# Performance work log

Hardware: AMD Instinct MI355X
Metric: run time of the kernel (lower is better)

## Reference

```python
import jax, jax.numpy as jnp
import numpy as np

N_NODES = 50000
N_EDGES = 800000
IN_CH = 256
HID = 512
NUM_LAYERS = 3
EPS = 1e-12  # F.normalize eps


def setup_inputs() -> dict:
    key = jax.random.key(0)
    ks = jax.random.split(key, 2 + 3 * NUM_LAYERS)
    x = jax.random.normal(ks[0], (N_NODES, IN_CH), dtype=jnp.float32)
    edge_index = jax.random.randint(ks[1], (2, N_EDGES), 0, N_NODES, dtype=jnp.int64)
    inp = {"x": x, "edge_index": edge_index}
    dims = [(IN_CH, HID)] + [(HID, HID)] * (NUM_LAYERS - 1)
    for i, (din, dout) in enumerate(dims):
        s = 1.0 / np.sqrt(din)
        inp[f"Wl{i}"] = jax.random.normal(ks[2 + 3 * i], (din, dout), dtype=jnp.float32) * s
        inp[f"bl{i}"] = jnp.zeros((dout,), dtype=jnp.float32)
        inp[f"Wr{i}"] = jax.random.normal(ks[3 + 3 * i], (din, dout), dtype=jnp.float32) * s
    return inp


def _sage_conv(x, src, dst, Wl, bl, Wr):
    # aggr='add': out[dst] += x[src], then lin_l(agg) + lin_r(x), L2 normalize rows
    agg = jax.ops.segment_sum(x[src], dst, num_segments=x.shape[0])  # [N, din]
    out = agg @ Wl + bl + x @ Wr  # [N, dout]
    norm = jnp.maximum(jnp.linalg.norm(out, axis=-1, keepdims=True), EPS)
    return out / norm


def reference(x, edge_index, Wl0, bl0, Wr0, Wl1, bl1, Wr1, Wl2, bl2, Wr2):
    src, dst = edge_index[0], edge_index[1]
    feat = x
    params = [(Wl0, bl0, Wr0), (Wl1, bl1, Wr1), (Wl2, bl2, Wr2)]
    for Wl, bl, Wr in params:
        aggre = _sage_conv(feat, src, dst, Wl, bl, Wr)
        # Dropout(p=0.15) is identity in eval mode
        feat = jax.nn.elu(aggre)
    return feat
```

## Files before the change

kernel.cpp:

```cpp
#include <hip/hip_runtime.h>
#include <math.h>

#define N_NODES 50000
#define M_PAD   50048
#define N_EDGES 800000
#define HID 512

typedef short bf16x8 __attribute__((ext_vector_type(8)));
typedef float f32x4  __attribute__((ext_vector_type(4)));
typedef unsigned short u16x4 __attribute__((ext_vector_type(4)));
typedef unsigned short u16x8 __attribute__((ext_vector_type(8)));

__device__ inline float b2f(unsigned short u) {
    union { unsigned int i; float f; } v; v.i = ((unsigned int)u) << 16; return v.f;
}
__device__ inline unsigned short f2b(float f) {
    union { float f; unsigned int i; } v; v.f = f;
    unsigned int r = v.i + 0x7FFFu + ((v.i >> 16) & 1u);
    return (unsigned short)(r >> 16);
}


__global__ void zero_kernel(int* __restrict__ p, int n) {
    int i = blockIdx.x * blockDim.x + threadIdx.x;
    if (i < n) p[i] = 0;
}

__global__ void detect_kernel(const int* __restrict__ e, int* __restrict__ flag) {
    if (blockIdx.x == 0 && threadIdx.x == 0) {
        int is64 = 1;
        for (int i = 0; i < 16; ++i)
            if (e[2 * i + 1] != 0) is64 = 0;
        *flag = is64;
    }
}

__global__ void hist_kernel(const void* __restrict__ eidx, const int* __restrict__ flag,
                            int* __restrict__ counts) {
    int e = blockIdx.x * blockDim.x + threadIdx.x;
    if (e >= N_EDGES) return;
    int is64 = *flag;
    int d;
    if (is64) d = (int)((const long long*)eidx)[N_EDGES + e];
    else      d = ((const int*)eidx)[N_EDGES + e];
    atomicAdd(&counts[d], 1);
}

__global__ __launch_bounds__(1024) void scan_kernel(const int* __restrict__ counts,
                                                    int* __restrict__ offsets) {
    __shared__ int sums[1024];
    int t = threadIdx.x;
    const int CH = (N_NODES + 1023) / 1024;
    int lo = t * CH;
    int hi = min(lo + CH, N_NODES);
    int s = 0;
    for (int i = lo; i < hi; ++i) s += counts[i];
    sums[t] = s;
    __syncthreads();
    for (int off = 1; off < 1024; off <<= 1) {
        int v = 0;
        if (t >= off) v = sums[t - off];
        __syncthreads();
        sums[t] += v;
        __syncthreads();
    }
    int excl = (t == 0) ? 0 : sums[t - 1];
    for (int i = lo; i < hi; ++i) { offsets[i] = excl; excl += counts[i]; }
    if (t == 1023) offsets[N_NODES] = excl;
}

__global__ void fill_kernel(const void* __restrict__ eidx, const int* __restrict__ flag,
                            const int* __restrict__ offsets, int* __restrict__ cursor,
                            int* __restrict__ edge_src) {
    int e = blockIdx.x * blockDim.x + threadIdx.x;
    if (e >= N_EDGES) return;
    int is64 = *flag;
    int s, d;
    if (is64) {
        const long long* p = (const long long*)eidx;
        s = (int)p[e];
        d = (int)p[N_EDGES + e];
    } else {
        const int* p = (const int*)eidx;
        s = p[e];
        d = p[N_EDGES + e];
    }
    int pos = atomicAdd(&cursor[d], 1);
    edge_src[offsets[d] + pos] = s;
}


__global__ __launch_bounds__(256) void xconv_kernel(const float* __restrict__ x,
                                                    unsigned short* __restrict__ cat1) {
    int id = blockIdx.x * 256 + threadIdx.x;
    if (id >= M_PAD * 64) return;
    int row = id >> 6;
    int c = (id & 63) * 4;
    float4 v = make_float4(0.f, 0.f, 0.f, 0.f);
    if (row < N_NODES) v = *(const float4*)(x + (size_t)row * 256 + c);
    ushort4 h;
    h.x = f2b(v.x); h.y = f2b(v.y); h.z = f2b(v.z); h.w = f2b(v.w);
    *(ushort4*)(cat1 + (size_t)row * 512 + 256 + c) = h;
}

__global__ __launch_bounds__(128) void wconv_kernel(const float* __restrict__ W,
                                                    unsigned short* __restrict__ T,
                                                    int K, int ktot, int off) {
    int n = blockIdx.x;
    for (int k = threadIdx.x; k < K; k += 128)
        T[(size_t)n * ktot + off + k] = f2b(W[(size_t)k * HID + n]);
}


template <int EPL>
__global__ __launch_bounds__(256) void aggregate_kernel(const unsigned short* __restrict__ Fh,
                                                        const int* __restrict__ off,
                                                        const int* __restrict__ esrc,
                                                        unsigned short* __restrict__ Ah) {
    const int STRIDE = 2 * EPL * 64;
    const int wid = threadIdx.x >> 6;
    const int lane = threadIdx.x & 63;
    const int node = blockIdx.x * 4 + wid;
    if (node >= N_NODES) return;
    const int beg = off[node], end = off[node + 1];
    const int deg = end - beg;
    const int lb = lane * EPL;
    using VecT = typename std::conditional<EPL == 8, u16x8, u16x4>::type;

    float a0[EPL], a1[EPL];
#pragma unroll
    for (int j = 0; j < EPL; ++j) { a0[j] = 0.f; a1[j] = 0.f; }

    int idxv = 0;
    int i = 0;
    for (; i + 8 <= deg; i += 8) {
        const int b = i & 63;
        if (b == 0) idxv = (beg + i + lane < end) ? esrc[beg + i + lane] : 0;
        int s[8];
#pragma unroll
        for (int k = 0; k < 8; ++k) s[k] = __shfl(idxv, b + k);
        VecT v[8];
#pragma unroll
        for (int k = 0; k < 8; ++k)
            v[k] = *(const VecT*)(Fh + (size_t)s[k] * STRIDE + lb);
#pragma unroll
        for (int k = 0; k < 8; ++k) {
#pragma unroll
            for (int j = 0; j < EPL; ++j) {
                if (k & 1) a1[j] += b2f(v[k][j]);
                else       a0[j] += b2f(v[k][j]);
            }
        }
    }
    for (; i < deg; ++i) {
        const int b = i & 63;
        if (b == 0) idxv = (beg + i + lane < end) ? esrc[beg + i + lane] : 0;
        const int s = __shfl(idxv, b);
        VecT v = *(const VecT*)(Fh + (size_t)s * STRIDE + lb);
#pragma unroll
        for (int j = 0; j < EPL; ++j) a0[j] += b2f(v[j]);
    }

    unsigned short* op = Ah + (size_t)node * STRIDE + lb;
    VecT h;
#pragma unroll
    for (int j = 0; j < EPL; ++j) h[j] = f2b(a0[j] + a1[j]);
    __builtin_nontemporal_store(h, (VecT*)op);
}


template <int FINAL>
__global__ __launch_bounds__(512, 2) void gemm_mfma_kernel(
    const unsigned short* __restrict__ A, const unsigned short* __restrict__ B,
    const float* __restrict__ bias, float* __restrict__ outF,
    unsigned short* __restrict__ pre, int K) {
    __shared__ unsigned short S[2 * 12288];
    const int bm = blockIdx.y * 128;
    const int bn = blockIdx.x * 256;
    const int tid = threadIdx.x;
    const int l = tid & 63;
    const int w = tid >> 6;
    const int wr = (w >> 2) * 64;
    const int wc = (w & 3) * 64;

    const int se = (tid >> 2) * 32 + (tid & 3) * 8;
    const unsigned short* gA  = A + (size_t)(bm + (tid >> 2)) * K + (tid & 3) * 8;
    const unsigned short* gB0 = B + (size_t)(bn + (tid >> 2)) * K + (tid & 3) * 8;
    const unsigned short* gB1 = B + (size_t)(bn + 128 + (tid >> 2)) * K + (tid & 3) * 8;

    f32x4 acc[4][4];
#pragma unroll
    for (int m = 0; m < 4; ++m)
#pragma unroll
        for (int n = 0; n < 4; ++n) acc[m][n] = (f32x4){0.f, 0.f, 0.f, 0.f};

    const int aoff = (wr + (l & 15)) * 32 + (l >> 4) * 8;
    const int woff = 4096 + (wc + (l & 15)) * 32 + (l >> 4) * 8;
    const int ktiles = K >> 5;

    auto STAGE = [&](int buf, int kt) {
        unsigned short* lb = &S[buf * 12288];
        __builtin_amdgcn_global_load_lds(
            (const __attribute__((address_space(1))) void*)(gA + kt * 32),
            (__attribute__((address_space(3))) void*)(lb + se), 16, 0, 0);
        __builtin_amdgcn_global_load_lds(
            (const __attribute__((address_space(1))) void*)(gB0 + kt * 32),
            (__attribute__((address_space(3))) void*)(lb + 4096 + se), 16, 0, 0);
        __builtin_amdgcn_global_load_lds(
            (const __attribute__((address_space(1))) void*)(gB1 + kt * 32),
            (__attribute__((address_space(3))) void*)(lb + 8192 + se), 16, 0, 0);
    };

    STAGE(0, 0);
    __syncthreads();

    for (int kt = 0; kt < ktiles; ++kt) {
        if (kt + 1 < ktiles) STAGE((kt + 1) & 1, kt + 1);
        const int sb = (kt & 1) * 12288;

        bf16x8 af[4], wf[4];
#pragma unroll
        for (int m = 0; m < 4; ++m)
            af[m] = *(const bf16x8*)&S[sb + aoff + m * 512];
#pragma unroll
        for (int n = 0; n < 4; ++n)
            wf[n] = *(const bf16x8*)&S[sb + woff + n * 512];
#pragma unroll
        for (int m = 0; m < 4; ++m)
#pragma unroll
            for (int n = 0; n < 4; ++n)
                acc[m][n] = __builtin_amdgcn_mfma_f32_16x16x32_bf16(af[m], wf[n], acc[m][n], 0, 0, 0);
        __syncthreads();
    }

    const int r0 = bm + wr + (l >> 4) * 4;
    const int c0 = bn + wc + (l & 15);
#pragma unroll
    for (int n = 0; n < 4; ++n) {
        const float bv = bias[c0 + n * 16];
#pragma unroll
        for (int m = 0; m < 4; ++m) {
#pragma unroll
            for (int j = 0; j < 4; ++j) {
                int gr = r0 + m * 16 + j;
                if (gr < N_NODES) {
                    float val = acc[m][n][j] + bv;
                    if constexpr (FINAL)
                        outF[(size_t)gr * HID + c0 + n * 16] = val;
                    else
                        pre[(size_t)gr * HID + c0 + n * 16] = f2b(val);
                }
            }
        }
    }
}


template <int FINAL>
__global__ __launch_bounds__(256) void norm_elu_kernel(const void* __restrict__ inp,
                                                       float* __restrict__ outF,
                                                       unsigned short* __restrict__ Fh) {
    const int wid = threadIdx.x >> 6;
    const int lane = threadIdx.x & 63;
    const int row = blockIdx.x * 4 + wid;
    if (row >= N_NODES) return;
    float r[8];
    if constexpr (FINAL) {
        const float* p = (const float*)inp + (size_t)row * HID + lane * 8;
        float4 v0 = *(const float4*)p;
        float4 v1 = *(const float4*)(p + 4);
        r[0] = v0.x; r[1] = v0.y; r[2] = v0.z; r[3] = v0.w;
        r[4] = v1.x; r[5] = v1.y; r[6] = v1.z; r[7] = v1.w;
    } else {
        const unsigned short* p = (const unsigned short*)inp + (size_t)row * HID + lane * 8;
        u16x8 v = *(const u16x8*)p;
#pragma unroll
        for (int j = 0; j < 8; ++j) r[j] = b2f(v[j]);
    }
    float ss = 0.f;
#pragma unroll
    for (int j = 0; j < 8; ++j) ss += r[j] * r[j];
#pragma unroll
    for (int o = 32; o > 0; o >>= 1) ss += __shfl_xor(ss, o);
    float inv = 1.f / fmaxf(sqrtf(ss), 1e-12f);
#pragma unroll
    for (int j = 0; j < 8; ++j) {
        r[j] *= inv;
        r[j] = r[j] > 0.f ? r[j] : expm1f(r[j]);
    }
    if constexpr (FINAL) {
        float* q = outF + (size_t)row * HID + lane * 8;
        *(float4*)q = make_float4(r[0], r[1], r[2], r[3]);
        *(float4*)(q + 4) = make_float4(r[4], r[5], r[6], r[7]);
    } else {
        unsigned short* q = Fh + (size_t)row * 1024 + lane * 8;
        u16x8 h;
#pragma unroll
        for (int j = 0; j < 8; ++j) h[j] = f2b(r[j]);
        *(u16x8*)q = h;
    }
}


extern "C" void kernel_launch(void* const* d_in, const int* in_sizes, int n_in,
                              void* d_out, int out_size, void* d_ws, size_t ws_size,
                              hipStream_t stream) {
    const float* x    = (const float*)d_in[0];
    const void*  eidx = d_in[1];
    const float* Wl0 = (const float*)d_in[2];
    const float* bl0 = (const float*)d_in[3];
    const float* Wr0 = (const float*)d_in[4];
    const float* Wl1 = (const float*)d_in[5];
    const float* bl1 = (const float*)d_in[6];
    const float* Wr1 = (const float*)d_in[7];
    const float* Wl2 = (const float*)d_in[8];
    const float* bl2 = (const float*)d_in[9];
    const float* Wr2 = (const float*)d_in[10];
    float* outF = (float*)d_out;
    unsigned short* preB = (unsigned short*)d_out;

    char* ws = (char*)d_ws;
    size_t o = 0;
    auto alloc = [&](size_t bytes) { void* p = ws + o; o += (bytes + 255) & ~(size_t)255; return p; };

    unsigned short* Cat1 = (unsigned short*)alloc((size_t)M_PAD * 512 * 2);
    unsigned short* Cat2 = (unsigned short*)alloc((size_t)M_PAD * 1024 * 2);

    unsigned short* Wcat0 = (unsigned short*)alloc(512 * 512 * 2);
    unsigned short* Wcat1 = (unsigned short*)alloc(512 * 1024 * 2);
    unsigned short* Wcat2 = (unsigned short*)alloc(512 * 1024 * 2);

    int* counts   = (int*)alloc((size_t)2 * N_NODES * 4);
    int* cursor   = counts + N_NODES;
    int* offsets  = (int*)alloc((size_t)(N_NODES + 1) * 4);
    int* edge_src = (int*)alloc((size_t)N_EDGES * 4);
    int* flag     = (int*)alloc(256);

    zero_kernel<<<(2 * N_NODES + 255) / 256, 256, 0, stream>>>(counts, 2 * N_NODES);
    detect_kernel<<<1, 64, 0, stream>>>((const int*)eidx, flag);
    hist_kernel<<<(N_EDGES + 255) / 256, 256, 0, stream>>>(eidx, flag, counts);
    scan_kernel<<<1, 1024, 0, stream>>>(counts, offsets);
    fill_kernel<<<(N_EDGES + 255) / 256, 256, 0, stream>>>(eidx, flag, offsets, cursor, edge_src);

    xconv_kernel<<<(M_PAD * 64 + 255) / 256, 256, 0, stream>>>(x, Cat1);
    wconv_kernel<<<512, 128, 0, stream>>>(Wl0, Wcat0, 256, 512, 0);
    wconv_kernel<<<512, 128, 0, stream>>>(Wr0, Wcat0, 256, 512, 256);
    wconv_kernel<<<512, 128, 0, stream>>>(Wl1, Wcat1, 512, 1024, 0);
    wconv_kernel<<<512, 128, 0, stream>>>(Wr1, Wcat1, 512, 1024, 512);
    wconv_kernel<<<512, 128, 0, stream>>>(Wl2, Wcat2, 512, 1024, 0);
    wconv_kernel<<<512, 128, 0, stream>>>(Wr2, Wcat2, 512, 1024, 512);

    dim3 ggrid(2, M_PAD / 128);
    const int ngrid = (N_NODES + 3) / 4;

    aggregate_kernel<4><<<ngrid, 256, 0, stream>>>(Cat1 + 256, offsets, edge_src, Cat1);
    gemm_mfma_kernel<0><<<ggrid, 512, 0, stream>>>(Cat1, Wcat0, bl0, nullptr, preB, 512);
    norm_elu_kernel<0><<<ngrid, 256, 0, stream>>>(preB, nullptr, Cat2 + 512);

    aggregate_kernel<8><<<ngrid, 256, 0, stream>>>(Cat2 + 512, offsets, edge_src, Cat2);
    gemm_mfma_kernel<0><<<ggrid, 512, 0, stream>>>(Cat2, Wcat1, bl1, nullptr, preB, 1024);
    norm_elu_kernel<0><<<ngrid, 256, 0, stream>>>(preB, nullptr, Cat2 + 512);

    aggregate_kernel<8><<<ngrid, 256, 0, stream>>>(Cat2 + 512, offsets, edge_src, Cat2);
    gemm_mfma_kernel<1><<<ggrid, 512, 0, stream>>>(Cat2, Wcat2, bl2, outF, nullptr, 1024);
    norm_elu_kernel<1><<<ngrid, 256, 0, stream>>>(outF, outF, nullptr);

    (void)in_sizes; (void)n_in; (void)out_size; (void)ws_size;
}
```

Before: 784.8 us.

## Split aggregation across column slices with one bf16 element per lane

The neighbor aggregation now uses a separate block for each 64-column slice of the feature row, so each lane gathers a single bf16 element per neighbor instead of a 4- or 8-element vector. The grid grows 4x or 8x, and the unroll drops from 8 to 4 neighbors with four independent accumulators. The aim is more parallelism and more loads in flight. The cost is 2-byte scalar gathers instead of 8- or 16-byte vector loads, and the edge index list is reread once per slice.

Result: slower. 919.1 us (+17.1%).

```diff
diff --git a/kernel.cpp b/kernel.cpp
--- a/kernel.cpp
+++ b/kernel.cpp
@@ -8,7 +8,6 @@
 
 typedef short bf16x8 __attribute__((ext_vector_type(8)));
 typedef float f32x4  __attribute__((ext_vector_type(4)));
-typedef unsigned short u16x4 __attribute__((ext_vector_type(4)));
 typedef unsigned short u16x8 __attribute__((ext_vector_type(8)));
 
 __device__ inline float b2f(unsigned short u) {
@@ -112,60 +111,44 @@
 }
 
 
-template <int EPL>
+template <int W>
 __global__ __launch_bounds__(256) void aggregate_kernel(const unsigned short* __restrict__ Fh,
                                                         const int* __restrict__ off,
                                                         const int* __restrict__ esrc,
                                                         unsigned short* __restrict__ Ah) {
-    const int STRIDE = 2 * EPL * 64;
+    const int NSLICE = W / 64;
+    const int STRIDE = 2 * W;
+    const int slice = blockIdx.x % NSLICE;
+    const int chunk = blockIdx.x / NSLICE;
     const int wid = threadIdx.x >> 6;
     const int lane = threadIdx.x & 63;
-    const int node = blockIdx.x * 4 + wid;
+    const int node = chunk * 4 + wid;
     if (node >= N_NODES) return;
     const int beg = off[node], end = off[node + 1];
     const int deg = end - beg;
-    const int lb = lane * EPL;
-    using VecT = typename std::conditional<EPL == 8, u16x8, u16x4>::type;
-
-    float a0[EPL], a1[EPL];
-#pragma unroll
-    for (int j = 0; j < EPL; ++j) { a0[j] = 0.f; a1[j] = 0.f; }
-
+    const int col = slice * 64 + lane;
+
+    float a0 = 0.f, a1 = 0.f, a2 = 0.f, a3 = 0.f;
     int idxv = 0;
     int i = 0;
-    for (; i + 8 <= deg; i += 8) {
+    for (; i + 4 <= deg; i += 4) {
         const int b = i & 63;
         if (b == 0) idxv = (beg + i + lane < end) ? esrc[beg + i + lane] : 0;
-        int s[8];
-#pragma unroll
-        for (int k = 0; k < 8; ++k) s[k] = __shfl(idxv, b + k);
-        VecT v[8];
-#pragma unroll
-        for (int k = 0; k < 8; ++k)
-            v[k] = *(const VecT*)(Fh + (size_t)s[k] * STRIDE + lb);
-#pragma unroll
-        for (int k = 0; k < 8; ++k) {
-#pragma unroll
-            for (int j = 0; j < EPL; ++j) {
-                if (k & 1) a1[j] += b2f(v[k][j]);
-                else       a0[j] += b2f(v[k][j]);
-            }
-        }
+        const int s0 = __shfl(idxv, b);
+        const int s1 = __shfl(idxv, b + 1);
+        const int s2 = __shfl(idxv, b + 2);
+        const int s3 = __shfl(idxv, b + 3);
+        a0 += b2f(Fh[(size_t)s0 * STRIDE + col]);
+        a1 += b2f(Fh[(size_t)s1 * STRIDE + col]);
+        a2 += b2f(Fh[(size_t)s2 * STRIDE + col]);
+        a3 += b2f(Fh[(size_t)s3 * STRIDE + col]);
     }
     for (; i < deg; ++i) {
         const int b = i & 63;
         if (b == 0) idxv = (beg + i + lane < end) ? esrc[beg + i + lane] : 0;
-        const int s = __shfl(idxv, b);
-        VecT v = *(const VecT*)(Fh + (size_t)s * STRIDE + lb);
-#pragma unroll
-        for (int j = 0; j < EPL; ++j) a0[j] += b2f(v[j]);
-    }
-
-    unsigned short* op = Ah + (size_t)node * STRIDE + lb;
-    VecT h;
-#pragma unroll
-    for (int j = 0; j < EPL; ++j) h[j] = f2b(a0[j] + a1[j]);
-    __builtin_nontemporal_store(h, (VecT*)op);
+        a0 += b2f(Fh[(size_t)__shfl(idxv, b) * STRIDE + col]);
+    }
+    Ah[(size_t)node * STRIDE + col] = f2b(a0 + a1 + a2 + a3);
 }
 
 
@@ -351,19 +334,19 @@
     wconv_kernel<<<512, 128, 0, stream>>>(Wr2, Wcat2, 512, 1024, 512);
 
     dim3 ggrid(2, M_PAD / 128);
-    const int ngrid = (N_NODES + 3) / 4;
-
-    aggregate_kernel<4><<<ngrid, 256, 0, stream>>>(Cat1 + 256, offsets, edge_src, Cat1);
+    const int nchunk = (N_NODES + 3) / 4;
+
+    aggregate_kernel<256><<<nchunk * 4, 256, 0, stream>>>(Cat1 + 256, offsets, edge_src, Cat1);
     gemm_mfma_kernel<0><<<ggrid, 512, 0, stream>>>(Cat1, Wcat0, bl0, nullptr, preB, 512);
-    norm_elu_kernel<0><<<ngrid, 256, 0, stream>>>(preB, nullptr, Cat2 + 512);
-
-    aggregate_kernel<8><<<ngrid, 256, 0, stream>>>(Cat2 + 512, offsets, edge_src, Cat2);
+    norm_elu_kernel<0><<<nchunk, 256, 0, stream>>>(preB, nullptr, Cat2 + 512);
+
+    aggregate_kernel<512><<<nchunk * 8, 256, 0, stream>>>(Cat2 + 512, offsets, edge_src, Cat2);
     gemm_mfma_kernel<0><<<ggrid, 512, 0, stream>>>(Cat2, Wcat1, bl1, nullptr, preB, 1024);
-    norm_elu_kernel<0><<<ngrid, 256, 0, stream>>>(preB, nullptr, Cat2 + 512);
-
-    aggregate_kernel<8><<<ngrid, 256, 0, stream>>>(Cat2 + 512, offsets, edge_src, Cat2);
+    norm_elu_kernel<0><<<nchunk, 256, 0, stream>>>(preB, nullptr, Cat2 + 512);
+
+    aggregate_kernel<512><<<nchunk * 8, 256, 0, stream>>>(Cat2 + 512, offsets, edge_src, Cat2);
     gemm_mfma_kernel<1><<<ggrid, 512, 0, stream>>>(Cat2, Wcat2, bl2, outF, nullptr, 1024);
-    norm_elu_kernel<1><<<ngrid, 256, 0, stream>>>(outF, outF, nullptr);
+    norm_elu_kernel<1><<<nchunk, 256, 0, stream>>>(outF, outF, nullptr);
 
     (void)in_sizes; (void)n_in; (void)out_size; (void)ws_size;
 }
```
